# Kernel tuning notes

Measured on AMD Instinct MI355X. Metric: run time of the kernel, lower is better.

The kernel has to match this reference:

```python
import jax, jax.numpy as jnp
import numpy as np

B = 512; Nt = 8; Nr = 8; Ld = 256; Lp = 16; qAry = 2
LDPC_N = qAry * Nt * Ld      # 4096
M_A = 3 * LDPC_N             # 12288
SQ2 = float(np.sqrt(2.0))


def setup_inputs() -> dict:
    key = jax.random.key(0)
    ks = jax.random.split(key, 12)
    # Sparse-ish binary ADMM expansion matrix A (rows = check-edge constraints)
    A = (jax.random.uniform(ks[0], (M_A, LDPC_N)) < 0.005).astype(jnp.float32)
    # Lambda_A ~ column weights of A (keeps the w denominator well behaved)
    Lambda_A = (jnp.sum(A, axis=0) + 1.0).reshape(LDPC_N, 1)
    theta = jax.random.uniform(ks[1], (M_A, 1), dtype=jnp.float32)
    sigma2_I = jnp.tile(0.1 * jnp.eye(2 * Nt, dtype=jnp.float32)[None], (B, 1, 1))
    return {
        "sigma2_I": sigma2_I,
        "Y": jax.random.normal(ks[2], (B, 2 * Nr, Ld), dtype=jnp.float32),
        "YYp": jax.random.normal(ks[3], (B, Nr, 2 * (Ld + Lp)), dtype=jnp.float32),
        "real_Xp": jax.random.normal(ks[4], (B, Nt, Lp), dtype=jnp.float32) / SQ2,
        "imag_Xp": jax.random.normal(ks[5], (B, Nt, Lp), dtype=jnp.float32) / SQ2,
        "lambda_W": jax.random.uniform(ks[6], (B, 1, 1), minval=0.5, maxval=1.5),
        "F": jax.random.normal(ks[7], (B, 2 * Nt, Ld), dtype=jnp.float32),
        "u": jax.random.uniform(ks[8], (B, LDPC_N, 1), dtype=jnp.float32),
        "z": jax.random.uniform(ks[9], (B, M_A, 1), dtype=jnp.float32),
        "lambda1": jax.random.uniform(ks[10], (B, M_A, 1), dtype=jnp.float32),
        "acc_new": jnp.zeros((B, 1, 1), dtype=jnp.float32),
        "A": A, "theta": theta, "Lambda_A": Lambda_A,
        "miu": jnp.full((1, 1), 0.6, dtype=jnp.float32),
        "alpha": jnp.full((1, 1), 11.0, dtype=jnp.float32),
        "factor": jnp.full((1, 1), 1.0, dtype=jnp.float32),
        "relax": jnp.full((1, 1), 1.0, dtype=jnp.float32),
        "acc": jnp.full((1, 1), 0.0, dtype=jnp.float32),
    }


def reference(sigma2_I, Y, YYp, real_Xp, imag_Xp, lambda_W, F, u, z, lambda1,
              acc_new, A, theta, Lambda_A, miu, alpha, factor, relax, acc):
    relu = jax.nn.relu
    z_old, lam_old = z, lambda1
    A_T = A.T
    # --- qAry == 2 detection update ---
    fb = 4.0 * lambda_W                                   # (B,1,1)
    # reorder F (B, 2Nt, Ld) into bit layout (B, 2*Nt*Ld, 1)
    res = F.transpose(0, 2, 1).reshape(-1, Ld, 2, Nt).transpose(0, 1, 3, 2)
    res = res.reshape(-1, 2 * Nt * Ld, 1)
    fb_res = 2.0 * lambda_W - 2.0 * SQ2 * res
    q = miu * jnp.matmul(A_T, theta - z - lambda1) + fb_res - alpha  # (B,LDPC_N,1)
    w = 1.0 / (miu * Lambda_A + fb - 2.0 * alpha)
    u = q * w
    u = relu(u) - relu(u - 1.0)                           # clip to [0,1]
    u_order = u.reshape(-1, Ld, Nt, qAry).transpose(0, 2, 1, 3)  # (B,Nt,Ld,2)
    real_X = (1.0 - 2.0 * u_order[:, :, :, 0]) / SQ2      # (B,Nt,Ld)
    imag_X = (1.0 - 2.0 * u_order[:, :, :, 1]) / SQ2
    X = jnp.concatenate([real_X, imag_X], axis=1)          # (B,2Nt,Ld)
    # --- MMSE channel re-estimation ---
    real_XXp = jnp.concatenate([real_X, real_Xp], axis=2)
    imag_XXp = jnp.concatenate([imag_X, imag_Xp], axis=2)
    XXp = jnp.concatenate([jnp.concatenate([real_XXp, imag_XXp], 2),
                           jnp.concatenate([-imag_XXp, real_XXp], 2)], 1)  # (B,2Nt,2(Ld+Lp))
    R = jnp.matmul(XXp, XXp.transpose(0, 2, 1)) + sigma2_I  # (B,2Nt,2Nt)
    inv_R = jnp.linalg.inv(R)
    W_temp = jnp.matmul(jnp.matmul(inv_R, XXp), YYp.transpose(0, 2, 1))  # (B,2Nt,Nr)
    real_W = W_temp[:, :Nt, :]
    imag_W = W_temp[:, Nt:2 * Nt, :]
    W = jnp.concatenate([jnp.concatenate([real_W, imag_W], 2),
                         jnp.concatenate([-imag_W, real_W], 2)], 1).transpose(0, 2, 1)  # (B,2Nr,2Nt)
    lambda_W = factor * lambda_W
    WT = W.transpose(0, 2, 1)
    F_new = jnp.matmul(WT, Y) + lambda_W * X - jnp.matmul(jnp.matmul(WT, W), X)
    # --- z / lambda1 ADMM update ---
    ztemp = theta - relax * jnp.matmul(A, u) - (1.0 - relax) * (theta - z_old) - lambda1
    z = relu(ztemp)
    lambda1 = -ztemp + z
    z = z + acc * (z - z_old)
    lambda1 = lambda1 + acc * (lambda1 - lam_old)
    return (lambda_W, F_new, u, z, lambda1, acc_new)
```

## Files before the change

### kernel.cpp

```cpp
#include <hip/hip_runtime.h>
#include <math.h>

#define BB 512
#define NT 8
#define NR 8
#define LDIM 256
#define LP 16
#define LDPC_N 4096
#define M_A 12288
#define COLCAP 128
#define ROWCAP 64
#define SQ2 1.41421356237309515f
#define INVSQ2 0.70710678118654752f

typedef unsigned short u16;
typedef unsigned int u32;

__device__ __forceinline__ float bflo(u32 u) { return __uint_as_float(u << 16); }
__device__ __forceinline__ float bfhi(u32 u) { return __uint_as_float(u & 0xffff0000u); }
__device__ __forceinline__ u16 f2bf(float f) {
  u32 b = __float_as_uint(f);
  return (u16)((b + 0x7fffu + ((b >> 16) & 1u)) >> 16);
}
__device__ __forceinline__ void add8(const uint4& v, float* a) {
  a[0] += bflo(v.x); a[1] += bfhi(v.x);
  a[2] += bflo(v.y); a[3] += bfhi(v.y);
  a[4] += bflo(v.z); a[5] += bfhi(v.z);
  a[6] += bflo(v.w); a[7] += bfhi(v.w);
}

__global__ __launch_bounds__(256) void build_sparse(
    const float* __restrict__ A, int* __restrict__ colcnt, int* __restrict__ rowcnt,
    int* __restrict__ csc_c, int* __restrict__ csr_c) {
  const long long total4 = (long long)M_A * LDPC_N / 4;
  long long stride = (long long)gridDim.x * blockDim.x;
  for (long long t = (long long)blockIdx.x * blockDim.x + threadIdx.x; t < total4; t += stride) {
    float4 a = ((const float4*)A)[t];
    long long base = t * 4;
    float av[4] = {a.x, a.y, a.z, a.w};
#pragma unroll
    for (int l = 0; l < 4; l++) {
      if (av[l] != 0.0f) {
        long long lin = base + l;
        int i = (int)(lin >> 12);
        int j = (int)(lin & 4095);
        int sc = atomicAdd(&colcnt[j], 1);
        if (sc < COLCAP) csc_c[j * COLCAP + sc] = i;
        int sr = atomicAdd(&rowcnt[i], 1);
        if (sr < ROWCAP) csr_c[i * ROWCAP + sr] = j;
      }
    }
  }
}

__global__ __launch_bounds__(256) void t1tf(
    const float* __restrict__ z, const float* __restrict__ lam,
    const float* __restrict__ theta, const float* __restrict__ F,
    u16* __restrict__ VT, u16* __restrict__ FT) {
  __shared__ float tile[256 * 33];
  int bx = blockIdx.x;
  if (bx < 6144) {
    int i0 = (bx % 384) * 32, b0 = (bx / 384) * 32;
    {
      int il = threadIdx.x & 31, bq = threadIdx.x >> 5;
      float th = theta[i0 + il];
#pragma unroll
      for (int m = 0; m < 4; m++) {
        int bl = bq + m * 8;
        size_t off = (size_t)(b0 + bl) * M_A + i0 + il;
        tile[il * 33 + bl] = th - z[off] - lam[off];
      }
    }
    __syncthreads();
    {
      int bl = threadIdx.x & 31, iq = threadIdx.x >> 5;
#pragma unroll
      for (int m = 0; m < 4; m++) {
        int il = iq + m * 8;
        VT[(size_t)(i0 + il) * BB + b0 + bl] = f2bf(tile[il * 33 + bl]);
      }
    }
  } else {
    int t = bx - 6144;
    int j0 = (t & 15) * 256, b0 = (t >> 4) * 32;
    int ld0 = j0 >> 4;
    int cc = threadIdx.x >> 4, dd = threadIdx.x & 15;
    int jl = dd * 16 + ((cc & 7) << 1) + (cc >> 3);
    for (int m = 0; m < 32; m++) {
      tile[jl * 33 + m] = F[(size_t)(b0 + m) * 4096 + cc * 256 + ld0 + dd];
    }
    __syncthreads();
    int bl = threadIdx.x & 31, jq = threadIdx.x >> 5;
    for (int jj = 0; jj < 32; jj++) {
      int jlo = jq * 32 + jj;
      FT[(size_t)(j0 + jlo) * BB + b0 + bl] = f2bf(tile[jlo * 33 + bl]);
    }
  }
}

__global__ __launch_bounds__(256) void k1_spmm(
    const u16* __restrict__ VT, const u16* __restrict__ FT,
    const int* __restrict__ colcnt, const int* __restrict__ csc_c,
    const float* __restrict__ lambda_W, const float* __restrict__ Lambda_A,
    const float* __restrict__ miu_p, const float* __restrict__ alpha_p,
    u16* __restrict__ UT) {
  __shared__ int idx[4 * COLCAP];
  __shared__ float lwS[512];
  __shared__ int cnts[4];
  __shared__ float lamA[4];
  int j0 = blockIdx.x * 4;
  int t = threadIdx.x;
  for (int s = t; s < 4 * COLCAP; s += 256) idx[s] = csc_c[j0 * COLCAP + s];
  for (int s = t; s < 512; s += 256) lwS[s] = lambda_W[s];
  if (t < 4) {
    cnts[t] = min(colcnt[j0 + t], COLCAP);
    lamA[t] = Lambda_A[j0 + t];
  }
  __syncthreads();
  int w = t >> 6, l = t & 63;
  int j = j0 + w;
  int boff = 8 * l;
  int cnt = cnts[w];
  const int* ic = &idx[w * COLCAP];
  float av[8] = {0, 0, 0, 0, 0, 0, 0, 0};
  int k = 0;
  for (; k + 1 < cnt; k += 2) {
    uint4 va = *(const uint4*)&VT[(size_t)ic[k] * BB + boff];
    uint4 vb = *(const uint4*)&VT[(size_t)ic[k + 1] * BB + boff];
    add8(va, av);
    add8(vb, av);
  }
  if (k < cnt) {
    uint4 va = *(const uint4*)&VT[(size_t)ic[k] * BB + boff];
    add8(va, av);
  }
  float miu = miu_p[0], alpha = alpha_p[0];
  float la = lamA[w];
  uint4 fr = *(const uint4*)&FT[(size_t)j * BB + boff];
  float res[8] = {bflo(fr.x), bfhi(fr.x), bflo(fr.y), bfhi(fr.y),
                  bflo(fr.z), bfhi(fr.z), bflo(fr.w), bfhi(fr.w)};
  u32 pk[4];
#pragma unroll
  for (int e = 0; e < 4; e++) {
    float lw0 = lwS[boff + 2 * e], lw1 = lwS[boff + 2 * e + 1];
    float q0 = miu * av[2 * e] + 2.0f * lw0 - 2.0f * SQ2 * res[2 * e] - alpha;
    float q1 = miu * av[2 * e + 1] + 2.0f * lw1 - 2.0f * SQ2 * res[2 * e + 1] - alpha;
    float w0 = 1.0f / (miu * la + 4.0f * lw0 - 2.0f * alpha);
    float w1 = 1.0f / (miu * la + 4.0f * lw1 - 2.0f * alpha);
    float u0 = fminf(fmaxf(q0 * w0, 0.0f), 1.0f);
    float u1 = fminf(fmaxf(q1 * w1, 0.0f), 1.0f);
    pk[e] = (u32)f2bf(u0) | ((u32)f2bf(u1) << 16);
  }
  *(uint4*)&UT[(size_t)j * BB + boff] = make_uint4(pk[0], pk[1], pk[2], pk[3]);
}

__global__ __launch_bounds__(256) void fused3(
    const u16* __restrict__ UT, const float* __restrict__ z_old,
    const float* __restrict__ lam_old, const float* __restrict__ theta,
    const float* __restrict__ relax_p, const float* __restrict__ acc_p,
    const int* __restrict__ rowcnt, const int* __restrict__ csr_c,
    float* __restrict__ out_u, float* __restrict__ out_z, float* __restrict__ out_lam,
    const float* __restrict__ real_Xp, const float* __restrict__ imag_Xp,
    const float* __restrict__ sigma2_I, const float* __restrict__ YYp,
    const float* __restrict__ Y, const float* __restrict__ lambda_W,
    const float* __restrict__ factor_p, const float* __restrict__ acc_new_in,
    float* __restrict__ out_lw, float* __restrict__ out_F, float* __restrict__ out_accnew) {
  __shared__ float smem[9856];
  int bidx = blockIdx.x;
  int tid = threadIdx.x;

  if (bidx < 2048) {
    float* tile = smem;
    int j0 = (bidx & 127) * 32, b0 = (bidx >> 7) * 32;
    {
      int bl = tid & 31, jq = tid >> 5;
#pragma unroll
      for (int m = 0; m < 4; m++) {
        int jl = jq + m * 8;
        tile[jl * 33 + bl] = bflo((u32)UT[(size_t)(j0 + jl) * BB + b0 + bl]);
      }
    }
    __syncthreads();
    {
      int jl = tid & 31, bq = tid >> 5;
#pragma unroll
      for (int m = 0; m < 4; m++) {
        int bl = bq + m * 8;
        out_u[(size_t)(b0 + bl) * LDPC_N + j0 + jl] = tile[jl * 33 + bl];
      }
    }
  } else if (bidx < 2816) {
    int* idx = (int*)smem;
    int* cnts = idx + 1024;
    float* ths = (float*)(idx + 1040);
    float* ssum = (float*)(idx + 1056);
    int i0 = (bidx - 2048) * 16;
    for (int s = tid; s < 1024; s += 256) idx[s] = csr_c[i0 * ROWCAP + s];
    if (tid < 16) {
      cnts[tid] = min(rowcnt[i0 + tid], ROWCAP);
      ths[tid] = theta[i0 + tid];
    }
    __syncthreads();
    int w = tid >> 6, l = tid & 63, boff = 8 * l;
    for (int rr = 0; rr < 4; rr++) {
      int r = w * 4 + rr;
      int cnt = cnts[r];
      const int* ir = &idx[r * ROWCAP];
      float s[8] = {0, 0, 0, 0, 0, 0, 0, 0};
      int k = 0;
      for (; k + 1 < cnt; k += 2) {
        uint4 va = *(const uint4*)&UT[(size_t)ir[k] * BB + boff];
        uint4 vb = *(const uint4*)&UT[(size_t)ir[k + 1] * BB + boff];
        add8(va, s);
        add8(vb, s);
      }
      if (k < cnt) {
        uint4 va = *(const uint4*)&UT[(size_t)ir[k] * BB + boff];
        add8(va, s);
      }
      *(float4*)&ssum[r * 520 + boff] = make_float4(s[0], s[1], s[2], s[3]);
      *(float4*)&ssum[r * 520 + boff + 4] = make_float4(s[4], s[5], s[6], s[7]);
    }
    __syncthreads();
    float relax = relax_p[0], acc = acc_p[0];
    int iw = tid & 15, bq = tid >> 4;
    float th = ths[iw];
    for (int p = 0; p < 32; p++) {
      int b = p * 16 + bq;
      size_t off = (size_t)b * M_A + i0 + iw;
      float zo = z_old[off];
      float lo = lam_old[off];
      float s = ssum[iw * 520 + b];
      float ztemp = th - relax * s - (1.0f - relax) * (th - zo) - lo;
      float zn = fmaxf(ztemp, 0.0f);
      float ln = zn - ztemp;
      out_z[off] = zn + acc * (zn - zo);
      out_lam[off] = ln + acc * (ln - lo);
    }
  } else {
    float* XX = smem;
    float* Rs = XX + 8720;
    float* invd = Rs + 272;
    float* Tm = invd + 16;
    float* Wcs = Tm + 128;
    float* Gs = Wcs + 256;
#define XXA(r, c) XX[(r) * 545 + (c)]
#define RLp(i, j) Rs[(i) * 17 + (j)]
    int b = bidx - 2816;

    for (int m = tid; m < 1024; m += 256) {
      int ld = m >> 2;
      int nt = (2 * m) & 7;
      int j4 = 4 * m;
      float q0 = bflo((u32)UT[(size_t)(j4 + 0) * BB + b]);
      float q1 = bflo((u32)UT[(size_t)(j4 + 1) * BB + b]);
      float q2 = bflo((u32)UT[(size_t)(j4 + 2) * BB + b]);
      float q3 = bflo((u32)UT[(size_t)(j4 + 3) * BB + b]);
      float vr0 = (1.0f - 2.0f * q0) * INVSQ2, vi0 = (1.0f - 2.0f * q1) * INVSQ2;
      float vr1 = (1.0f - 2.0f * q2) * INVSQ2, vi1 = (1.0f - 2.0f * q3) * INVSQ2;
      XXA(nt, ld) = vr0;          XXA(nt, 272 + ld) = vi0;
      XXA(8 + nt, ld) = -vi0;     XXA(8 + nt, 272 + ld) = vr0;
      XXA(nt + 1, ld) = vr1;      XXA(nt + 1, 272 + ld) = vi1;
      XXA(9 + nt, ld) = -vi1;     XXA(9 + nt, 272 + ld) = vr1;
    }
    if (tid < 128) {
      int r = tid >> 4, pc = tid & 15;
      float vr = real_Xp[(size_t)b * 128 + tid];
      float vi = imag_Xp[(size_t)b * 128 + tid];
      XXA(r, 256 + pc) = vr;       XXA(r, 528 + pc) = vi;
      XXA(8 + r, 256 + pc) = -vi;  XXA(8 + r, 528 + pc) = vr;
    }
    __syncthreads();

    for (int p = tid; p < 264; p += 256) {
      if (p < 136) {
        int i = 0;
        while ((i + 1) * (i + 2) / 2 <= p) i++;
        int jj = p - i * (i + 1) / 2;
        float s = 0.0f;
        for (int k = 0; k < 544; k++) s += XXA(i, k) * XXA(jj, k);
        RLp(i, jj) = s + sigma2_I[(size_t)b * 256 + i * 16 + jj];
      } else {
        int q = p - 136;
        int i = q >> 3, m = q & 7;
        const float* yb = YYp + (size_t)b * 4352 + m * 544;
        float s = 0.0f;
        for (int k = 0; k < 544; k++) s += XXA(i, k) * yb[k];
        Tm[i * 8 + m] = s;
      }
    }
    __syncthreads();

    for (int k = 0; k < 16; k++) {
      if (tid == 0) {
        float d = sqrtf(fmaxf(RLp(k, k), 1e-30f));
        RLp(k, k) = d;
        invd[k] = 1.0f / d;
      }
      __syncthreads();
      if (tid > k && tid < 16) RLp(tid, k) *= invd[k];
      __syncthreads();
      {
        int i = tid >> 4, jj = tid & 15;
        if (i > k && jj > k && jj <= i) RLp(i, jj) -= RLp(i, k) * RLp(jj, k);
      }
      __syncthreads();
    }

    if (tid < 8) {
      int m = tid;
      float yv[16], wv[16];
#pragma unroll
      for (int r = 0; r < 16; r++) {
        float s = Tm[r * 8 + m];
        for (int c = 0; c < r; c++) s -= RLp(r, c) * yv[c];
        yv[r] = s * invd[r];
      }
#pragma unroll
      for (int r = 15; r >= 0; r--) {
        float s = yv[r];
        for (int c = r + 1; c < 16; c++) s -= RLp(c, r) * wv[c];
        wv[r] = s * invd[r];
      }
#pragma unroll
      for (int r = 0; r < 16; r++) Tm[r * 8 + m] = wv[r];
    }
    __syncthreads();

    {
      int i = tid >> 4, jj = tid & 15;
      int ii = i & 7, jc = jj & 7;
      float val;
      if (i < 8) val = (jj < 8) ? Tm[ii * 8 + jc] : Tm[(8 + ii) * 8 + jc];
      else       val = (jj < 8) ? -Tm[(8 + ii) * 8 + jc] : Tm[ii * 8 + jc];
      Wcs[tid] = val;
    }
    __syncthreads();
    {
      int i = tid >> 4, jj = tid & 15;
      float s = 0.0f;
#pragma unroll
      for (int k = 0; k < 16; k++) s += Wcs[i * 16 + k] * Wcs[jj * 16 + k];
      Gs[tid] = s;
    }
    __syncthreads();

    float lw_new = factor_p[0] * lambda_W[b];
    {
      int ld = tid;
      float Xv[16], Yv[16];
#pragma unroll
      for (int c = 0; c < 8; c++) {
        Xv[c] = XXA(c, ld);
        Xv[8 + c] = XXA(c, 272 + ld);
      }
      const float* Yb = Y + (size_t)b * 16 * LDIM;
#pragma unroll
      for (int c = 0; c < 16; c++) Yv[c] = Yb[c * LDIM + ld];
      float* Fb = out_F + (size_t)b * 16 * LDIM;
      for (int r = 0; r < 16; r++) {
        float s = lw_new * Xv[r];
#pragma unroll
        for (int c = 0; c < 16; c++) s += Wcs[r * 16 + c] * Yv[c] - Gs[r * 16 + c] * Xv[c];
        Fb[r * LDIM + ld] = s;
      }
    }
    if (tid == 0) {
      out_lw[b] = lw_new;
      out_accnew[b] = acc_new_in[b];
    }
#undef XXA
#undef RLp
  }
}

extern "C" void kernel_launch(void* const* d_in, const int* in_sizes, int n_in,
                              void* d_out, int out_size, void* d_ws, size_t ws_size,
                              hipStream_t stream) {
  const float* sigma2_I  = (const float*)d_in[0];
  const float* Y         = (const float*)d_in[1];
  const float* YYp       = (const float*)d_in[2];
  const float* real_Xp   = (const float*)d_in[3];
  const float* imag_Xp   = (const float*)d_in[4];
  const float* lambda_W  = (const float*)d_in[5];
  const float* F         = (const float*)d_in[6];
  const float* z         = (const float*)d_in[8];
  const float* lam       = (const float*)d_in[9];
  const float* acc_new_i = (const float*)d_in[10];
  const float* A         = (const float*)d_in[11];
  const float* theta     = (const float*)d_in[12];
  const float* Lambda_A  = (const float*)d_in[13];
  const float* miu       = (const float*)d_in[14];
  const float* alpha     = (const float*)d_in[15];
  const float* factor    = (const float*)d_in[16];
  const float* relax     = (const float*)d_in[17];
  const float* acc       = (const float*)d_in[18];

  float* out = (float*)d_out;
  float* out_lw     = out;
  float* out_F      = out_lw + BB;
  float* out_u      = out_F + (size_t)BB * 2 * NT * LDIM;
  float* out_z      = out_u + (size_t)BB * LDPC_N;
  float* out_lam    = out_z + (size_t)BB * M_A;
  float* out_accnew = out_lam + (size_t)BB * M_A;

  u16* VT = (u16*)out_z;
  u16* FT = (u16*)out_lam;

  int* ws = (int*)d_ws;
  int* colcnt = ws;
  int* rowcnt = colcnt + LDPC_N;
  int* csc_c  = rowcnt + M_A;
  int* csr_c  = csc_c + COLCAP * LDPC_N;
  u16* UT     = (u16*)(csr_c + ROWCAP * M_A);

  hipMemsetAsync(colcnt, 0, (LDPC_N + M_A) * sizeof(int), stream);
  build_sparse<<<2048, 256, 0, stream>>>(A, colcnt, rowcnt, csc_c, csr_c);
  t1tf<<<6400, 256, 0, stream>>>(z, lam, theta, F, VT, FT);
  k1_spmm<<<LDPC_N / 4, 256, 0, stream>>>(VT, FT, colcnt, csc_c, lambda_W,
                                          Lambda_A, miu, alpha, UT);
  fused3<<<3328, 256, 0, stream>>>(UT, z, lam, theta, relax, acc, rowcnt, csr_c,
                                   out_u, out_z, out_lam,
                                   real_Xp, imag_Xp, sigma2_I, YYp, Y, lambda_W,
                                   factor, acc_new_i, out_lw, out_F, out_accnew);
}
```

Baseline: 505.8 us.

## Merge sparse build and transpose kernels, specialize ADMM update, vectorize Gram dot products

Merges the sparse-index build kernel and the transpose/bf16 conversion kernel into one launch so the atomic scan of A overlaps with the z/lam and F transposes. The F transpose tile shrinks to 16 batches, halving its shared memory and doubling its block count. The z/lambda epilogue gets a fast path when relax==1 and acc==0 that skips loading z_old. The Gram and cross-correlation dot products pad the XX row stride to 548 and read it with float4 loads. The fast path depends on runtime scalar values, and the padding changes the shared-memory layout.

```diff
diff --git a/kernel.cpp b/kernel.cpp
--- a/kernel.cpp
+++ b/kernel.cpp
@@ -29,40 +29,40 @@
   a[6] += bflo(v.w); a[7] += bfhi(v.w);
 }
 
-__global__ __launch_bounds__(256) void build_sparse(
+__global__ __launch_bounds__(256) void prep(
     const float* __restrict__ A, int* __restrict__ colcnt, int* __restrict__ rowcnt,
-    int* __restrict__ csc_c, int* __restrict__ csr_c) {
-  const long long total4 = (long long)M_A * LDPC_N / 4;
-  long long stride = (long long)gridDim.x * blockDim.x;
-  for (long long t = (long long)blockIdx.x * blockDim.x + threadIdx.x; t < total4; t += stride) {
-    float4 a = ((const float4*)A)[t];
-    long long base = t * 4;
-    float av[4] = {a.x, a.y, a.z, a.w};
-#pragma unroll
-    for (int l = 0; l < 4; l++) {
-      if (av[l] != 0.0f) {
-        long long lin = base + l;
-        int i = (int)(lin >> 12);
-        int j = (int)(lin & 4095);
-        int sc = atomicAdd(&colcnt[j], 1);
-        if (sc < COLCAP) csc_c[j * COLCAP + sc] = i;
-        int sr = atomicAdd(&rowcnt[i], 1);
-        if (sr < ROWCAP) csr_c[i * ROWCAP + sr] = j;
-      }
-    }
-  }
-}
-
-__global__ __launch_bounds__(256) void t1tf(
+    int* __restrict__ csc_c, int* __restrict__ csr_c,
     const float* __restrict__ z, const float* __restrict__ lam,
     const float* __restrict__ theta, const float* __restrict__ F,
     u16* __restrict__ VT, u16* __restrict__ FT) {
-  __shared__ float tile[256 * 33];
+  __shared__ float tile[256 * 17];
   int bx = blockIdx.x;
-  if (bx < 6144) {
-    int i0 = (bx % 384) * 32, b0 = (bx / 384) * 32;
-    {
-      int il = threadIdx.x & 31, bq = threadIdx.x >> 5;
+  int tid = threadIdx.x;
+  if (bx < 2048) {
+    const long long total4 = (long long)M_A * LDPC_N / 4;
+    const long long stride = 2048LL * 256LL;
+    for (long long t = (long long)bx * 256 + tid; t < total4; t += stride) {
+      float4 a = ((const float4*)A)[t];
+      long long base = t * 4;
+      float av[4] = {a.x, a.y, a.z, a.w};
+#pragma unroll
+      for (int l = 0; l < 4; l++) {
+        if (av[l] != 0.0f) {
+          long long lin = base + l;
+          int i = (int)(lin >> 12);
+          int j = (int)(lin & 4095);
+          int sc = atomicAdd(&colcnt[j], 1);
+          if (sc < COLCAP) csc_c[j * COLCAP + sc] = i;
+          int sr = atomicAdd(&rowcnt[i], 1);
+          if (sr < ROWCAP) csr_c[i * ROWCAP + sr] = j;
+        }
+      }
+    }
+  } else if (bx < 8192) {
+    int bx2 = bx - 2048;
+    int i0 = (bx2 % 384) * 32, b0 = (bx2 / 384) * 32;
+    {
+      int il = tid & 31, bq = tid >> 5;
       float th = theta[i0 + il];
 #pragma unroll
       for (int m = 0; m < 4; m++) {
@@ -73,7 +73,7 @@
     }
     __syncthreads();
     {
-      int bl = threadIdx.x & 31, iq = threadIdx.x >> 5;
+      int bl = tid & 31, iq = tid >> 5;
 #pragma unroll
       for (int m = 0; m < 4; m++) {
         int il = iq + m * 8;
@@ -81,19 +81,19 @@
       }
     }
   } else {
-    int t = bx - 6144;
-    int j0 = (t & 15) * 256, b0 = (t >> 4) * 32;
+    int bx3 = bx - 8192;
+    int j0 = (bx3 & 15) * 256, b0 = (bx3 >> 4) * 16;
     int ld0 = j0 >> 4;
-    int cc = threadIdx.x >> 4, dd = threadIdx.x & 15;
+    int cc = tid >> 4, dd = tid & 15;
     int jl = dd * 16 + ((cc & 7) << 1) + (cc >> 3);
-    for (int m = 0; m < 32; m++) {
-      tile[jl * 33 + m] = F[(size_t)(b0 + m) * 4096 + cc * 256 + ld0 + dd];
-    }
-    __syncthreads();
-    int bl = threadIdx.x & 31, jq = threadIdx.x >> 5;
-    for (int jj = 0; jj < 32; jj++) {
-      int jlo = jq * 32 + jj;
-      FT[(size_t)(j0 + jlo) * BB + b0 + bl] = f2bf(tile[jlo * 33 + bl]);
+    for (int m = 0; m < 16; m++) {
+      tile[jl * 17 + m] = F[(size_t)(b0 + m) * 4096 + cc * 256 + ld0 + dd];
+    }
+    __syncthreads();
+    int bl = tid & 15, jq = tid >> 4;
+    for (int jj = 0; jj < 16; jj++) {
+      int jlo = jq * 16 + jj;
+      FT[(size_t)(j0 + jlo) * BB + b0 + bl] = f2bf(tile[jlo * 17 + bl]);
     }
   }
 }
@@ -165,7 +165,7 @@
     const float* __restrict__ Y, const float* __restrict__ lambda_W,
     const float* __restrict__ factor_p, const float* __restrict__ acc_new_in,
     float* __restrict__ out_lw, float* __restrict__ out_F, float* __restrict__ out_accnew) {
-  __shared__ float smem[9856];
+  __shared__ float smem[9696];
   int bidx = blockIdx.x;
   int tid = threadIdx.x;
 
@@ -225,26 +225,38 @@
     float relax = relax_p[0], acc = acc_p[0];
     int iw = tid & 15, bq = tid >> 4;
     float th = ths[iw];
-    for (int p = 0; p < 32; p++) {
-      int b = p * 16 + bq;
-      size_t off = (size_t)b * M_A + i0 + iw;
-      float zo = z_old[off];
-      float lo = lam_old[off];
-      float s = ssum[iw * 520 + b];
-      float ztemp = th - relax * s - (1.0f - relax) * (th - zo) - lo;
-      float zn = fmaxf(ztemp, 0.0f);
-      float ln = zn - ztemp;
-      out_z[off] = zn + acc * (zn - zo);
-      out_lam[off] = ln + acc * (ln - lo);
+    if (relax == 1.0f && acc == 0.0f) {
+      for (int p = 0; p < 32; p++) {
+        int b = p * 16 + bq;
+        size_t off = (size_t)b * M_A + i0 + iw;
+        float lo = lam_old[off];
+        float ztemp = th - ssum[iw * 520 + b] - lo;
+        float zn = fmaxf(ztemp, 0.0f);
+        out_z[off] = zn;
+        out_lam[off] = zn - ztemp;
+      }
+    } else {
+      for (int p = 0; p < 32; p++) {
+        int b = p * 16 + bq;
+        size_t off = (size_t)b * M_A + i0 + iw;
+        float zo = z_old[off];
+        float lo = lam_old[off];
+        float s = ssum[iw * 520 + b];
+        float ztemp = th - relax * s - (1.0f - relax) * (th - zo) - lo;
+        float zn = fmaxf(ztemp, 0.0f);
+        float ln = zn - ztemp;
+        out_z[off] = zn + acc * (zn - zo);
+        out_lam[off] = ln + acc * (ln - lo);
+      }
     }
   } else {
     float* XX = smem;
-    float* Rs = XX + 8720;
+    float* Rs = XX + 8768;
     float* invd = Rs + 272;
     float* Tm = invd + 16;
     float* Wcs = Tm + 128;
     float* Gs = Wcs + 256;
-#define XXA(r, c) XX[(r) * 545 + (c)]
+#define XXA(r, c) XX[(r) * 548 + (c)]
 #define RLp(i, j) Rs[(i) * 17 + (j)]
     int b = bidx - 2816;
 
@@ -272,20 +284,29 @@
     }
     __syncthreads();
 
+    const float4* XX4 = (const float4*)XX;
     for (int p = tid; p < 264; p += 256) {
       if (p < 136) {
         int i = 0;
         while ((i + 1) * (i + 2) / 2 <= p) i++;
         int jj = p - i * (i + 1) / 2;
         float s = 0.0f;
-        for (int k = 0; k < 544; k++) s += XXA(i, k) * XXA(jj, k);
+        for (int k4 = 0; k4 < 136; k4++) {
+          float4 a = XX4[i * 137 + k4];
+          float4 c = XX4[jj * 137 + k4];
+          s += a.x * c.x + a.y * c.y + a.z * c.z + a.w * c.w;
+        }
         RLp(i, jj) = s + sigma2_I[(size_t)b * 256 + i * 16 + jj];
       } else {
         int q = p - 136;
         int i = q >> 3, m = q & 7;
-        const float* yb = YYp + (size_t)b * 4352 + m * 544;
+        const float4* yb4 = (const float4*)(YYp + (size_t)b * 4352 + m * 544);
         float s = 0.0f;
-        for (int k = 0; k < 544; k++) s += XXA(i, k) * yb[k];
+        for (int k4 = 0; k4 < 136; k4++) {
+          float4 a = XX4[i * 137 + k4];
+          float4 c = yb4[k4];
+          s += a.x * c.x + a.y * c.y + a.z * c.z + a.w * c.w;
+        }
         Tm[i * 8 + m] = s;
       }
     }
@@ -415,8 +436,8 @@
   u16* UT     = (u16*)(csr_c + ROWCAP * M_A);
 
   hipMemsetAsync(colcnt, 0, (LDPC_N + M_A) * sizeof(int), stream);
-  build_sparse<<<2048, 256, 0, stream>>>(A, colcnt, rowcnt, csc_c, csr_c);
-  t1tf<<<6400, 256, 0, stream>>>(z, lam, theta, F, VT, FT);
+  prep<<<8704, 256, 0, stream>>>(A, colcnt, rowcnt, csc_c, csr_c,
+                                 z, lam, theta, F, VT, FT);
   k1_spmm<<<LDPC_N / 4, 256, 0, stream>>>(VT, FT, colcnt, csc_c, lambda_W,
                                           Lambda_A, miu, alpha, UT);
   fused3<<<3328, 256, 0, stream>>>(UT, z, lam, theta, relax, acc, rowcnt, csr_c,
```

Measured after the change: 488.6 us. -3.4%, faster.
